# Optimization experiments

Measured on AMD Instinct MI355X. Metric: run time of the kernel, lower is better.

Reference implementation:

```python
import jax, jax.numpy as jnp
import numpy as np

SEQ_LEN = 2048
VOCAB = 32000
N_EMBD = 768
D_INNER = 1536
D_STATE = 16
D_CONV = 4
DT_RANK = 48
N_LAYERS = 2
EPS = 1e-5


def setup_inputs() -> dict:
    key = jax.random.key(0)
    ks = jax.random.split(key, 10)
    s = 0.02
    tokens = jax.random.randint(ks[0], (SEQ_LEN,), 0, VOCAB)
    E = jax.random.normal(ks[1], (VOCAB, N_EMBD)) * s  # tied embedding / lm_head
    in_proj_w = jax.random.normal(ks[2], (N_LAYERS, 2 * D_INNER, N_EMBD)) * s
    conv_w = jax.random.normal(ks[3], (N_LAYERS, D_INNER, 1, D_CONV)) * s  # depthwise
    conv_b = jax.random.normal(ks[4], (N_LAYERS, D_INNER)) * s
    x_proj_w = jax.random.normal(ks[5], (N_LAYERS, DT_RANK + 2 * D_STATE, D_INNER)) * s
    dt_proj_w = jax.random.normal(ks[6], (N_LAYERS, D_INNER, DT_RANK)) * s
    dt_proj_b = jax.random.normal(ks[7], (N_LAYERS, D_INNER)) * s
    # A init exactly as in the module: repeat(arange(1,d_state+1), d_inner).reshape(d_inner, d_state)
    A = jnp.repeat(jnp.arange(1, D_STATE + 1), D_INNER).reshape(D_INNER, D_STATE).astype(jnp.float32)
    A_log = jnp.broadcast_to(jnp.log(A), (N_LAYERS, D_INNER, D_STATE))
    D_param = jnp.ones((N_LAYERS, D_INNER))
    out_proj_w = jax.random.normal(ks[8], (N_LAYERS, N_EMBD, D_INNER)) * s
    norm_w = jnp.ones((N_LAYERS, N_EMBD))
    norm_b = jnp.zeros((N_LAYERS, N_EMBD))
    normf_w = jnp.ones((N_EMBD,))
    normf_b = jnp.zeros((N_EMBD,))
    return {
        'tokens': tokens, 'E': E, 'in_proj_w': in_proj_w, 'conv_w': conv_w,
        'conv_b': conv_b, 'x_proj_w': x_proj_w, 'dt_proj_w': dt_proj_w,
        'dt_proj_b': dt_proj_b, 'A_log': A_log, 'D_param': D_param,
        'out_proj_w': out_proj_w, 'norm_w': norm_w, 'norm_b': norm_b,
        'normf_w': normf_w, 'normf_b': normf_b,
    }


def _rmsnorm(x, w, b):
    inv = jax.lax.rsqrt(jnp.mean(x * x, axis=-1, keepdims=True) + EPS)
    return x * inv * w + b


def _selective_scan(u, delta, A, B, C, D):
    # u,delta: [L, d_inner]; A: [d_inner, d_state]; B,C: [L, d_state]; D: [d_inner]
    dA = jnp.exp(jnp.einsum('ld,dn->ldn', delta, A))            # [L, d_inner, d_state]
    dBu = (delta * u)[:, :, None] * B[:, None, :]               # [L, d_inner, d_state]

    def step(x, inp):
        dA_t, dBu_t, C_t = inp
        x = dA_t * x + dBu_t
        y = x @ C_t                                             # [d_inner]
        return x, y

    x0 = jnp.zeros((D_INNER, D_STATE), dtype=u.dtype)
    _, ys = jax.lax.scan(step, x0, (dA, dBu, C))
    return ys + u * D


def _mamba_block(xn, in_w, cw, cb, xp_w, dt_w, dt_b, a_log, d_p, out_w):
    L = xn.shape[0]
    x_and_res = xn @ in_w.T                                     # [L, 2*d_inner]
    x, res = jnp.split(x_and_res, 2, axis=-1)
    # depthwise causal conv with padding d_conv-1 (both sides), then crop to L
    xc = jax.lax.conv_general_dilated(
        x.T[None], cw, window_strides=(1,), padding=[(D_CONV - 1, D_CONV - 1)],
        feature_group_count=D_INNER, dimension_numbers=('NCH', 'OIH', 'NCH'))[0]
    x = (xc[:, :L] + cb[:, None]).T                             # [L, d_inner]
    x = jax.nn.silu(x)
    # ssm
    A = -jnp.exp(a_log)
    x_dbl = x @ xp_w.T                                          # [L, dt_rank + 2*d_state]
    delta, B, C = jnp.split(x_dbl, [DT_RANK, DT_RANK + D_STATE], axis=-1)
    delta = jax.nn.softplus(delta @ dt_w.T + dt_b)              # [L, d_inner]
    y = _selective_scan(x, delta, A, B, C, d_p)
    y = y * jax.nn.silu(res)
    return y @ out_w.T                                          # [L, n_embd]


def reference(tokens, E, in_proj_w, conv_w, conv_b, x_proj_w, dt_proj_w,
              dt_proj_b, A_log, D_param, out_proj_w, norm_w, norm_b,
              normf_w, normf_b):
    h = E[tokens]                                               # [L, n_embd]
    for i in range(N_LAYERS):
        h = h + _mamba_block(_rmsnorm(h, norm_w[i], norm_b[i]),
                             in_proj_w[i], conv_w[i], conv_b[i], x_proj_w[i],
                             dt_proj_w[i], dt_proj_b[i], A_log[i], D_param[i],
                             out_proj_w[i])
    h = _rmsnorm(h, normf_w, normf_b)
    logits = h @ E.T                                            # tied lm head
    return logits
```

## Files before the change

kernel.cpp:

```cpp
#include <hip/hip_runtime.h>
#include <hip/hip_bf16.h>

#define SEQ   2048
#define NE    768
#define DI    1536
#define DS    16
#define DC    4
#define DTR   48
#define NL    2
#define VOCAB 32000
#define EPS   1e-5f
#define CHUNK 128
#define NCH   (SEQ / CHUNK)

typedef __hip_bfloat16 bf16;
typedef __bf16 bf16x8 __attribute__((ext_vector_type(8)));
typedef float  f32x4  __attribute__((ext_vector_type(4)));

#define GLOBAL_AS __attribute__((address_space(1)))
#define LDS_AS    __attribute__((address_space(3)))

__device__ __forceinline__ void gload16(const void* g, void* l)
{
    __builtin_amdgcn_global_load_lds((const GLOBAL_AS void*)g, (LDS_AS void*)l, 16, 0, 0);
}

__global__ __launch_bounds__(256) void f2b_k(const float* __restrict__ x,
    bf16* __restrict__ y, int n)
{
    int i = (blockIdx.x * 256 + threadIdx.x) * 4;
    if (i >= n) return;
    float4 v = *reinterpret_cast<const float4*>(x + i);
    y[i + 0] = __float2bfloat16(v.x);
    y[i + 1] = __float2bfloat16(v.y);
    y[i + 2] = __float2bfloat16(v.z);
    y[i + 3] = __float2bfloat16(v.w);
}

__global__ __launch_bounds__(256) void embed_k(const int* __restrict__ tok,
    const float* __restrict__ E, float* __restrict__ h)
{
    int l = blockIdx.x;
    int t = tok[l];
    for (int k = threadIdx.x; k < NE; k += 256)
        h[(size_t)l * NE + k] = E[(size_t)t * NE + k];
}

__global__ __launch_bounds__(256) void rmsnorm_k(const float* __restrict__ x,
    const float* __restrict__ w, const float* __restrict__ b, bf16* __restrict__ out)
{
    int l = blockIdx.x;
    const float* xr = x + (size_t)l * NE;
    float ss = 0.f;
    for (int k = threadIdx.x; k < NE; k += 256) { float v = xr[k]; ss += v * v; }
    for (int o = 32; o; o >>= 1) ss += __shfl_down(ss, o);
    __shared__ float s4[4];
    if ((threadIdx.x & 63) == 0) s4[threadIdx.x >> 6] = ss;
    __syncthreads();
    float inv = rsqrtf((s4[0] + s4[1] + s4[2] + s4[3]) / NE + EPS);
    for (int k = threadIdx.x; k < NE; k += 256)
        out[(size_t)l * NE + k] = __float2bfloat16(xr[k] * inv * w[k] + b[k]);
}

__global__ __launch_bounds__(256) void gemm_bt(const bf16* __restrict__ Abf,
    const bf16* __restrict__ Bbf, float* __restrict__ Cout, int M, int N, int K,
    int accum)
{
    __shared__ __align__(16) __bf16 As[128 * 32];
    __shared__ __align__(16) __bf16 Bs[128 * 32];

    const int nwg = gridDim.x;
    const int bid = blockIdx.x;
    const int q = nwg >> 3, r = nwg & 7;
    const int xcd = bid & 7, loc = bid >> 3;
    const int swz = (xcd < r ? xcd * (q + 1) : r * (q + 1) + (xcd - r) * q) + loc;
    const int mb = M >> 7;
    const int npan = swz / mb;
    const int mpan = swz - npan * mb;
    const int tm = mpan * 128;
    const int tn = npan * 128;

    const int tid  = threadIdx.x;
    const int wave = tid >> 6;
    const int lane = tid & 63;
    const int wm = wave >> 1, wn = wave & 1;
    const int r16 = lane & 15, quad = lane >> 4;

    const __bf16* A = reinterpret_cast<const __bf16*>(Abf);
    const __bf16* B = reinterpret_cast<const __bf16*>(Bbf);

    const int c0 = tid, c1 = tid + 256;
    const __bf16* ga0 = A + (size_t)(tm + (c0 >> 2)) * K + (c0 & 3) * 8;
    const __bf16* ga1 = A + (size_t)(tm + (c1 >> 2)) * K + (c1 & 3) * 8;
    const __bf16* gb0 = B + (size_t)(tn + (c0 >> 2)) * K + (c0 & 3) * 8;
    const __bf16* gb1 = B + (size_t)(tn + (c1 >> 2)) * K + (c1 & 3) * 8;
    __bf16* la0 = As + c0 * 8;
    __bf16* la1 = As + c1 * 8;
    __bf16* lb0 = Bs + c0 * 8;
    __bf16* lb1 = Bs + c1 * 8;

    f32x4 zero = {0.f, 0.f, 0.f, 0.f};
    f32x4 acc[4][4];
#pragma unroll
    for (int i = 0; i < 4; i++)
#pragma unroll
        for (int j = 0; j < 4; j++) acc[i][j] = zero;

    const int arow = wm * 64 + r16;
    const int brow = wn * 64 + r16;

    for (int kt = 0; kt < K; kt += 32) {
        __syncthreads();
        gload16(ga0 + kt, la0);
        gload16(ga1 + kt, la1);
        gload16(gb0 + kt, lb0);
        gload16(gb1 + kt, lb1);
        __syncthreads();

        bf16x8 av[4], bv[4];
#pragma unroll
        for (int i = 0; i < 4; i++)
            av[i] = *reinterpret_cast<const bf16x8*>(As + (arow + i * 16) * 32 + quad * 8);
#pragma unroll
        for (int j = 0; j < 4; j++)
            bv[j] = *reinterpret_cast<const bf16x8*>(Bs + (brow + j * 16) * 32 + quad * 8);
#pragma unroll
        for (int i = 0; i < 4; i++)
#pragma unroll
            for (int j = 0; j < 4; j++)
                acc[i][j] = __builtin_amdgcn_mfma_f32_16x16x32_bf16(av[i], bv[j], acc[i][j], 0, 0, 0);
    }

#pragma unroll
    for (int i = 0; i < 4; i++) {
        int cm0 = tm + wm * 64 + i * 16 + quad * 4;
#pragma unroll
        for (int j = 0; j < 4; j++) {
            int cn = tn + wn * 64 + j * 16 + r16;
            if (accum) {
#pragma unroll
                for (int rr = 0; rr < 4; rr++)
                    Cout[(size_t)(cm0 + rr) * N + cn] += acc[i][j][rr];
            } else {
#pragma unroll
                for (int rr = 0; rr < 4; rr++)
                    Cout[(size_t)(cm0 + rr) * N + cn] = acc[i][j][rr];
            }
        }
    }
}

__global__ __launch_bounds__(256) void conv_silu_k(const float* __restrict__ xr,
    const float* __restrict__ cw, const float* __restrict__ cb, float* __restrict__ u)
{
    int idx = blockIdx.x * 256 + threadIdx.x;
    int l = idx / DI, d = idx - l * DI;
    float s = cb[d];
#pragma unroll
    for (int t = 0; t < DC; t++) {
        int ls = l - (DC - 1) + t;
        if (ls >= 0) s += xr[(size_t)ls * (2 * DI) + d] * cw[d * DC + t];
    }
    u[idx] = s / (1.f + expf(-s));
}

__global__ __launch_bounds__(256) void xproj_k(const float* __restrict__ u,
    const float* __restrict__ xpw, float* __restrict__ xdbl)
{
    int gw = blockIdx.x * 4 + (threadIdx.x >> 6);
    int l = gw / 80, j = gw - l * 80;
    int lane = threadIdx.x & 63;
    const float4* ur = reinterpret_cast<const float4*>(u + (size_t)l * DI);
    const float4* wr = reinterpret_cast<const float4*>(xpw + (size_t)j * DI);
    float s = 0.f;
#pragma unroll
    for (int k = lane; k < DI / 4; k += 64) {
        float4 a = ur[k], b = wr[k];
        s += a.x * b.x + a.y * b.y + a.z * b.z + a.w * b.w;
    }
    for (int o = 32; o; o >>= 1) s += __shfl_down(s, o);
    if (lane == 0) xdbl[(size_t)l * 80 + j] = s;
}

__global__ __launch_bounds__(256) void dtproj_k(const float* __restrict__ xdbl,
    const float* __restrict__ dtw, const float* __restrict__ dtb, float* __restrict__ delta)
{
    int d = blockIdx.x * 256 + threadIdx.x;
    float w[DTR];
    const float* wr = dtw + (size_t)d * DTR;
#pragma unroll
    for (int k = 0; k < DTR; k++) w[k] = wr[k];
    float bv = dtb[d];
    __shared__ float xs[DTR];
    int l0 = blockIdx.y * 32;
    for (int li = 0; li < 32; li++) {
        int l = l0 + li;
        __syncthreads();
        if (threadIdx.x < DTR) xs[threadIdx.x] = xdbl[(size_t)l * 80 + threadIdx.x];
        __syncthreads();
        float s = bv;
#pragma unroll
        for (int k = 0; k < DTR; k++) s += xs[k] * w[k];
        delta[(size_t)l * DI + d] = fmaxf(s, 0.f) + log1pf(expf(-fabsf(s)));
    }
}

__global__ __launch_bounds__(256) void scan1_k(const float* __restrict__ delta,
    const float* __restrict__ u, const float* __restrict__ xdbl,
    const float* __restrict__ alog, float* __restrict__ S, float* __restrict__ P)
{
    int dg = threadIdx.x >> 4, n = threadIdx.x & 15;
    int d = blockIdx.x * 16 + dg;
    int c = blockIdx.y;
    float A = -expf(alog[(size_t)d * DS + n]);
    float st = 0.f, pr = 1.f;
    int l0 = c * CHUNK;
#pragma unroll 4
    for (int t = 0; t < CHUNK; t++) {
        int l = l0 + t;
        float dl = delta[(size_t)l * DI + d];
        float ul = u[(size_t)l * DI + d];
        float Bn = xdbl[(size_t)l * 80 + DTR + n];
        float a = expf(dl * A);
        st = a * st + dl * ul * Bn;
        pr *= a;
    }
    size_t o = ((size_t)c * DI + d) * DS + n;
    S[o] = st;
    P[o] = pr;
}

__global__ __launch_bounds__(256) void scan2_k(const float* __restrict__ S,
    const float* __restrict__ P, float* __restrict__ sin_)
{
    int i = blockIdx.x * 256 + threadIdx.x;
    float run = 0.f;
#pragma unroll
    for (int c = 0; c < NCH; c++) {
        size_t o = (size_t)c * DI * DS + i;
        sin_[o] = run;
        run = S[o] + P[o] * run;
    }
}

__global__ __launch_bounds__(256) void scan3_k(const float* __restrict__ delta,
    const float* __restrict__ u, const float* __restrict__ xdbl,
    const float* __restrict__ alog, const float* __restrict__ sin_,
    const float* __restrict__ Dp, const float* __restrict__ xr,
    bf16* __restrict__ ybf)
{
    int dg = threadIdx.x >> 4, n = threadIdx.x & 15;
    int d = blockIdx.x * 16 + dg;
    int c = blockIdx.y;
    float A = -expf(alog[(size_t)d * DS + n]);
    float Dv = Dp[d];
    float st = sin_[((size_t)c * DI + d) * DS + n];
    int l0 = c * CHUNK;
#pragma unroll 2
    for (int t = 0; t < CHUNK; t++) {
        int l = l0 + t;
        float dl = delta[(size_t)l * DI + d];
        float ul = u[(size_t)l * DI + d];
        float Bn = xdbl[(size_t)l * 80 + DTR + n];
        float Cn = xdbl[(size_t)l * 80 + DTR + DS + n];
        float a = expf(dl * A);
        st = a * st + dl * ul * Bn;
        float p = st * Cn;
        p += __shfl_down(p, 8);
        p += __shfl_down(p, 4);
        p += __shfl_down(p, 2);
        p += __shfl_down(p, 1);
        if (n == 0) {
            float r = xr[(size_t)l * (2 * DI) + DI + d];
            float yv = (p + ul * Dv) * (r / (1.f + expf(-r)));
            ybf[(size_t)l * DI + d] = __float2bfloat16(yv);
        }
    }
}

extern "C" void kernel_launch(void* const* d_in, const int* in_sizes, int n_in,
                              void* d_out, int out_size, void* d_ws, size_t ws_size,
                              hipStream_t stream)
{
    const int*   tokens  = (const int*)  d_in[0];
    const float* E       = (const float*)d_in[1];
    const float* in_w    = (const float*)d_in[2];
    const float* conv_w  = (const float*)d_in[3];
    const float* conv_b  = (const float*)d_in[4];
    const float* xp_w    = (const float*)d_in[5];
    const float* dt_w    = (const float*)d_in[6];
    const float* dt_b    = (const float*)d_in[7];
    const float* A_log   = (const float*)d_in[8];
    const float* D_p     = (const float*)d_in[9];
    const float* out_w   = (const float*)d_in[10];
    const float* norm_w  = (const float*)d_in[11];
    const float* norm_b  = (const float*)d_in[12];
    const float* normf_w = (const float*)d_in[13];
    const float* normf_b = (const float*)d_in[14];

    char* ws = (char*)d_ws;
    size_t off = 0;
    auto alloc = [&](size_t bytes) -> void* {
        void* p = ws + off;
        off = (off + bytes + 255) & ~(size_t)255;
        return p;
    };

    float* h     = (float*)alloc((size_t)SEQ * NE * 4);
    bf16*  xn    = (bf16*) alloc((size_t)SEQ * NE * 2);
    float* xr    = (float*)alloc((size_t)SEQ * 2 * DI * 4);
    float* u     = (float*)alloc((size_t)SEQ * DI * 4);
    float* xdbl  = (float*)alloc((size_t)SEQ * 80 * 4);
    float* delta = (float*)alloc((size_t)SEQ * DI * 4);
    bf16*  ybf   = (bf16*) alloc((size_t)SEQ * DI * 2);
    bf16*  hf    = (bf16*) alloc((size_t)SEQ * NE * 2);
    bf16*  Ebf   = (bf16*) alloc((size_t)VOCAB * NE * 2);
    bf16*  wbuf  = (bf16*) alloc((size_t)2 * DI * NE * 2);
    float* Sbuf  = (float*)alloc((size_t)NCH * DI * DS * 4);
    float* Pbuf  = (float*)alloc((size_t)NCH * DI * DS * 4);
    float* Sin   = (float*)alloc((size_t)NCH * DI * DS * 4);

    {
        int n = VOCAB * NE;
        f2b_k<<<(n / 4 + 255) / 256, 256, 0, stream>>>(E, Ebf, n);
    }

    embed_k<<<SEQ, 256, 0, stream>>>(tokens, E, h);

    for (int L = 0; L < NL; L++) {
        rmsnorm_k<<<SEQ, 256, 0, stream>>>(h, norm_w + (size_t)L * NE, norm_b + (size_t)L * NE, xn);

        {
            int n = 2 * DI * NE;
            f2b_k<<<(n / 4 + 255) / 256, 256, 0, stream>>>(in_w + (size_t)L * n, wbuf, n);
        }
        gemm_bt<<<(2 * DI / 128) * (SEQ / 128), 256, 0, stream>>>(
            xn, wbuf, xr, SEQ, 2 * DI, NE, 0);

        conv_silu_k<<<SEQ * DI / 256, 256, 0, stream>>>(
            xr, conv_w + (size_t)L * DI * DC, conv_b + (size_t)L * DI, u);

        xproj_k<<<SEQ * 80 / 4, 256, 0, stream>>>(u, xp_w + (size_t)L * 80 * DI, xdbl);

        dtproj_k<<<dim3(DI / 256, SEQ / 32), 256, 0, stream>>>(
            xdbl, dt_w + (size_t)L * DI * DTR, dt_b + (size_t)L * DI, delta);

        const float* alog = A_log + (size_t)L * DI * DS;
        scan1_k<<<dim3(DI / 16, NCH), 256, 0, stream>>>(delta, u, xdbl, alog, Sbuf, Pbuf);
        scan2_k<<<DI * DS / 256, 256, 0, stream>>>(Sbuf, Pbuf, Sin);
        scan3_k<<<dim3(DI / 16, NCH), 256, 0, stream>>>(
            delta, u, xdbl, alog, Sin, D_p + (size_t)L * DI, xr, ybf);

        {
            int n = NE * DI;
            f2b_k<<<(n / 4 + 255) / 256, 256, 0, stream>>>(out_w + (size_t)L * n, wbuf, n);
        }
        gemm_bt<<<(NE / 128) * (SEQ / 128), 256, 0, stream>>>(
            ybf, wbuf, h, SEQ, NE, DI, 1);
    }

    rmsnorm_k<<<SEQ, 256, 0, stream>>>(h, normf_w, normf_b, hf);

    gemm_bt<<<(VOCAB / 128) * (SEQ / 128), 256, 0, stream>>>(
        hf, Ebf, (float*)d_out, SEQ, VOCAB, NE, 0);
}
```

Measured before the change: 1.194 ms.

## Add 256x256 pipelined MFMA GEMM for LM head and restructure xproj

Adds a new 512-thread GEMM kernel with 256x256 tiles, double-buffered LDS loads issued through global_load_lds, swizzled LDS layout, XCD-aware block remapping, and explicit waitcnt/barrier scheduling with setprio around the MFMA groups. It replaces the 128x128 GEMM for the large vocabulary projection, the dominant cost, to raise data reuse and overlap loads with compute. Separately, xproj now runs one block per token, staging the u row in shared memory and having each wave compute 20 outputs, instead of reloading u for every output. The hand-tuned barrier schedule is fragile, and the new GEMM relies on M, N and K being multiples of 256 and 128.

```diff
diff --git a/kernel.cpp b/kernel.cpp
--- a/kernel.cpp
+++ b/kernel.cpp
@@ -25,6 +25,12 @@
     __builtin_amdgcn_global_load_lds((const GLOBAL_AS void*)g, (LDS_AS void*)l, 16, 0, 0);
 }
 
+#define BAR()   __builtin_amdgcn_s_barrier()
+#define LGKM0() do { asm volatile("s_waitcnt lgkmcnt(0)" ::: "memory"); \
+                     __builtin_amdgcn_sched_barrier(0); } while (0)
+#define VMW(n)  do { asm volatile("s_waitcnt vmcnt(" #n ")" ::: "memory"); \
+                     __builtin_amdgcn_sched_barrier(0); } while (0)
+
 __global__ __launch_bounds__(256) void f2b_k(const float* __restrict__ x,
     bf16* __restrict__ y, int n)
 {
@@ -150,6 +156,176 @@
     }
 }
 
+__device__ __forceinline__ void ld_a_set(const __bf16* ldsp, int base, int s,
+    int r16, int quad, bf16x8 av[4][2])
+{
+    const int sw = (r16 & 4) << 2;
+#pragma unroll
+    for (int m = 0; m < 4; m++) {
+        const int row = s * 64 + m * 16 + r16;
+#pragma unroll
+        for (int kk = 0; kk < 2; kk++) {
+            const int off = base + row * 64 + ((kk * 32 + quad * 8) ^ sw);
+            av[m][kk] = *reinterpret_cast<const bf16x8*>(ldsp + off);
+        }
+    }
+}
+
+__device__ __forceinline__ void ld_b_set(const __bf16* ldsp, int base, int rowbase,
+    int nh, int r16, int quad, bf16x8 bv[2][2])
+{
+    const int sw = (r16 & 4) << 2;
+#pragma unroll
+    for (int n = 0; n < 2; n++) {
+        const int row = rowbase + nh * 32 + n * 16 + r16;
+#pragma unroll
+        for (int kk = 0; kk < 2; kk++) {
+            const int off = base + row * 64 + ((kk * 32 + quad * 8) ^ sw);
+            bv[n][kk] = *reinterpret_cast<const bf16x8*>(ldsp + off);
+        }
+    }
+}
+
+#define MFMA_Q(AV, S, NH)                                                        \
+    do {                                                                         \
+        __builtin_amdgcn_s_setprio(1);                                           \
+        _Pragma("unroll")                                                        \
+        for (int m = 0; m < 4; m++)                                              \
+            _Pragma("unroll")                                                    \
+            for (int n = 0; n < 2; n++)                                          \
+                _Pragma("unroll")                                                \
+                for (int kk = 0; kk < 2; kk++)                                   \
+                    acc[(S) * 4 + m][(NH) * 2 + n] =                             \
+                        __builtin_amdgcn_mfma_f32_16x16x32_bf16(                 \
+                            AV[m][kk], bv[n][kk],                                \
+                            acc[(S) * 4 + m][(NH) * 2 + n], 0, 0, 0);            \
+        __builtin_amdgcn_s_setprio(0);                                           \
+    } while (0)
+
+__global__ __launch_bounds__(512, 2) void gemm256(const bf16* __restrict__ Abf,
+    const bf16* __restrict__ Bbf, float* __restrict__ Cout, int M, int N, int K)
+{
+    __shared__ __align__(16) __bf16 lds[2 * 32768];
+
+    const int tid  = threadIdx.x;
+    const int wid  = tid >> 6;
+    const int lane = tid & 63;
+    const int wr = wid >> 2, wc = wid & 3;
+    const int r16 = lane & 15, quad = lane >> 4;
+
+    const int nwg = gridDim.x;
+    const int bid = blockIdx.x;
+    const int q = nwg >> 3, r = nwg & 7;
+    const int xcd = bid & 7, loc = bid >> 3;
+    const int swz = (xcd < r ? xcd * (q + 1) : r * (q + 1) + (xcd - r) * q) + loc;
+    const int mb = M >> 8;
+    const int npan = swz / mb;
+    const int mpan = swz - npan * mb;
+    const int tm = mpan * 256;
+    const int tn = npan * 256;
+
+    const __bf16* A = reinterpret_cast<const __bf16*>(Abf);
+    const __bf16* B = reinterpret_cast<const __bf16*>(Bbf);
+
+    const int ra = tid >> 3;
+    const int ca = ((tid & 7) * 8) ^ ((ra & 4) << 2);
+
+    auto stA = [&](int h, int t, int b) {
+        const __bf16* s0 = A + (size_t)(tm + h * 128 + ra) * K + t * 64 + ca;
+        __bf16* d = lds + b * 32768 + h * 8192;
+        gload16(s0, d + tid * 8);
+        gload16(s0 + (size_t)64 * K, d + (tid + 512) * 8);
+    };
+    auto stB = [&](int h, int t, int b) {
+        const __bf16* s0 = B + (size_t)(tn + h * 128 + ra) * K + t * 64 + ca;
+        __bf16* d = lds + b * 32768 + 16384 + h * 8192;
+        gload16(s0, d + tid * 8);
+        gload16(s0 + (size_t)64 * K, d + (tid + 512) * 8);
+    };
+
+    const int abase0 = wr * 8192;
+    const int abase1 = 32768 + wr * 8192;
+    const int bbase0 = 16384 + (wc >> 1) * 8192;
+    const int bbase1 = 32768 + 16384 + (wc >> 1) * 8192;
+    const int browb  = (wc & 1) * 64;
+
+    f32x4 zero = {0.f, 0.f, 0.f, 0.f};
+    f32x4 acc[8][4];
+#pragma unroll
+    for (int i = 0; i < 8; i++)
+#pragma unroll
+        for (int j = 0; j < 4; j++) acc[i][j] = zero;
+
+    bf16x8 av0[4][2], av1[4][2], bv[2][2];
+
+    const int NIT = K >> 7;
+
+    stA(0, 0, 0); stA(1, 0, 0); stB(0, 0, 0); stB(1, 0, 0);
+    stA(0, 1, 1); stA(1, 1, 1); stB(0, 1, 1);
+    VMW(6);
+    BAR();
+
+    for (int it = 0; it < NIT; ++it) {
+        const int t1 = 2 * it + 1, u0 = 2 * it + 2, u1 = 2 * it + 3;
+        const bool pf = (it + 1 < NIT);
+        ld_a_set(lds, abase0, 0, r16, quad, av0);
+        ld_b_set(lds, bbase0, browb, 0, r16, quad, bv);
+        stB(1, t1, 1);
+        BAR(); LGKM0();
+        MFMA_Q(av0, 0, 0);
+        BAR();
+        ld_a_set(lds, abase0, 1, r16, quad, av1);
+        BAR(); LGKM0();
+        MFMA_Q(av1, 1, 0);
+        BAR();
+        ld_b_set(lds, bbase0, browb, 1, r16, quad, bv);
+        if (pf) { stA(0, u0, 0); stA(1, u0, 0); }
+        BAR(); LGKM0();
+        MFMA_Q(av1, 1, 1);
+        BAR();
+        if (pf) stB(0, u0, 0);
+        if (pf) { VMW(6); } else { VMW(0); }
+        BAR(); LGKM0();
+        MFMA_Q(av0, 0, 1);
+        BAR();
+        ld_a_set(lds, abase1, 0, r16, quad, av0);
+        ld_b_set(lds, bbase1, browb, 0, r16, quad, bv);
+        if (pf) stB(1, u0, 0);
+        BAR(); LGKM0();
+        MFMA_Q(av0, 0, 0);
+        BAR();
+        ld_a_set(lds, abase1, 1, r16, quad, av1);
+        BAR(); LGKM0();
+        MFMA_Q(av1, 1, 0);
+        BAR();
+        ld_b_set(lds, bbase1, browb, 1, r16, quad, bv);
+        if (pf) { stA(0, u1, 1); stA(1, u1, 1); }
+        BAR(); LGKM0();
+        MFMA_Q(av1, 1, 1);
+        BAR();
+        if (pf) { stB(0, u1, 1); VMW(6); }
+        BAR(); LGKM0();
+        MFMA_Q(av0, 0, 1);
+        BAR();
+    }
+
+#pragma unroll
+    for (int s = 0; s < 2; s++)
+#pragma unroll
+        for (int m = 0; m < 4; m++) {
+            int cm0 = tm + wr * 128 + s * 64 + m * 16 + quad * 4;
+#pragma unroll
+            for (int nh = 0; nh < 2; nh++)
+#pragma unroll
+                for (int n = 0; n < 2; n++) {
+                    int cn = tn + wc * 64 + nh * 32 + n * 16 + r16;
+#pragma unroll
+                    for (int rr = 0; rr < 4; rr++)
+                        Cout[(size_t)(cm0 + rr) * N + cn] = acc[s * 4 + m][nh * 2 + n][rr];
+                }
+        }
+}
+
 __global__ __launch_bounds__(256) void conv_silu_k(const float* __restrict__ xr,
     const float* __restrict__ cw, const float* __restrict__ cb, float* __restrict__ u)
 {
@@ -167,19 +343,27 @@
 __global__ __launch_bounds__(256) void xproj_k(const float* __restrict__ u,
     const float* __restrict__ xpw, float* __restrict__ xdbl)
 {
-    int gw = blockIdx.x * 4 + (threadIdx.x >> 6);
-    int l = gw / 80, j = gw - l * 80;
-    int lane = threadIdx.x & 63;
+    __shared__ float us[DI];
+    int l = blockIdx.x;
     const float4* ur = reinterpret_cast<const float4*>(u + (size_t)l * DI);
-    const float4* wr = reinterpret_cast<const float4*>(xpw + (size_t)j * DI);
-    float s = 0.f;
-#pragma unroll
-    for (int k = lane; k < DI / 4; k += 64) {
-        float4 a = ur[k], b = wr[k];
-        s += a.x * b.x + a.y * b.y + a.z * b.z + a.w * b.w;
-    }
-    for (int o = 32; o; o >>= 1) s += __shfl_down(s, o);
-    if (lane == 0) xdbl[(size_t)l * 80 + j] = s;
+#pragma unroll
+    for (int k = threadIdx.x; k < DI / 4; k += 256)
+        *reinterpret_cast<float4*>(&us[k * 4]) = ur[k];
+    __syncthreads();
+    int w = threadIdx.x >> 6, lane = threadIdx.x & 63;
+    for (int jj = 0; jj < 20; jj++) {
+        int j = w * 20 + jj;
+        const float4* wr4 = reinterpret_cast<const float4*>(xpw + (size_t)j * DI);
+        float s = 0.f;
+#pragma unroll
+        for (int k = lane; k < DI / 4; k += 64) {
+            float4 a = *reinterpret_cast<const float4*>(&us[k * 4]);
+            float4 b = wr4[k];
+            s += a.x * b.x + a.y * b.y + a.z * b.z + a.w * b.w;
+        }
+        for (int o = 32; o; o >>= 1) s += __shfl_down(s, o);
+        if (lane == 0) xdbl[(size_t)l * 80 + j] = s;
+    }
 }
 
 __global__ __launch_bounds__(256) void dtproj_k(const float* __restrict__ xdbl,
@@ -340,7 +524,7 @@
         conv_silu_k<<<SEQ * DI / 256, 256, 0, stream>>>(
             xr, conv_w + (size_t)L * DI * DC, conv_b + (size_t)L * DI, u);
 
-        xproj_k<<<SEQ * 80 / 4, 256, 0, stream>>>(u, xp_w + (size_t)L * 80 * DI, xdbl);
+        xproj_k<<<SEQ, 256, 0, stream>>>(u, xp_w + (size_t)L * 80 * DI, xdbl);
 
         dtproj_k<<<dim3(DI / 256, SEQ / 32), 256, 0, stream>>>(
             xdbl, dt_w + (size_t)L * DI * DTR, dt_b + (size_t)L * DI, delta);
@@ -361,6 +545,6 @@
 
     rmsnorm_k<<<SEQ, 256, 0, stream>>>(h, normf_w, normf_b, hf);
 
-    gemm_bt<<<(VOCAB / 128) * (SEQ / 128), 256, 0, stream>>>(
-        hf, Ebf, (float*)d_out, SEQ, VOCAB, NE, 0);
-}
+    gemm256<<<(VOCAB / 256) * (SEQ / 256), 512, 0, stream>>>(
+        hf, Ebf, (float*)d_out, SEQ, VOCAB, NE);
+}
```

Measured after the change: 1.169 ms. 2.1% less time.
